# Performance work log

Hardware: AMD Instinct MI355X
Metric: run time of the kernel (lower is better)

The kernel has to match this reference:

```python
import jax, jax.numpy as jnp
import numpy as np

N_NODES = 400      # total nodes across batch
B = 10             # graphs in batch (40 nodes each)
N_CONFIGS = 1000   # fixed by tile dataset
CONFIG_FEAT_DIM = 24
NODE_FEAT_DIM = 85  # continuous cols; node_feat has +1 col for shape-ele-type idx
N_SHAPE_TYPES = 8
SHAPE_EMB = 4
N_OPS = 120
OP_EMB = 32
H = 64             # h_dim
E = 800            # edges
CAT_DIM = NODE_FEAT_DIM + SHAPE_EMB + OP_EMB + CONFIG_FEAT_DIM  # 145


def _lin(k, i, o):
    return jax.random.normal(k, (i, o), jnp.float32) * (1.0 / np.sqrt(i))


def setup_inputs() -> dict:
    key = jax.random.key(0)
    ks = jax.random.split(key, 32)
    node_cont = jax.random.normal(ks[0], (N_NODES, NODE_FEAT_DIM), jnp.float32)
    shape_type = jax.random.randint(ks[1], (N_NODES, 1), 0, N_SHAPE_TYPES).astype(jnp.float32)
    node_feat = jnp.concatenate([node_cont, shape_type], axis=-1)  # [N, 86]
    node_opcode = jax.random.randint(ks[2], (N_NODES,), 0, N_OPS)
    config_feat = jax.random.normal(ks[3], (B * N_CONFIGS, CONFIG_FEAT_DIM), jnp.float32)
    edge_index = jax.random.randint(ks[4], (2, E), 0, N_NODES)
    batch = jnp.arange(N_NODES) // (N_NODES // B)  # 40 nodes per graph
    inp = dict(
        node_feat=node_feat, node_opcode=node_opcode, config_feat=config_feat,
        edge_index=edge_index, batch=batch,
        op_emb=jax.random.normal(ks[5], (N_OPS, OP_EMB), jnp.float32),
        shape_emb=jax.random.normal(ks[6], (N_SHAPE_TYPES, SHAPE_EMB), jnp.float32),
        W1=_lin(ks[7], CAT_DIM, 2 * H), b1=jnp.zeros((2 * H,), jnp.float32),
        W2=_lin(ks[8], 2 * H, 2 * H), b2=jnp.zeros((2 * H,), jnp.float32),
        Wl0=_lin(ks[9], 2 * H, H), Wr0=_lin(ks[10], 2 * H, H), bg0=jnp.zeros((H,), jnp.float32),
        Wl1=_lin(ks[11], H, H), Wr1=_lin(ks[12], H, H), bg1=jnp.zeros((H,), jnp.float32),
        Wl2=_lin(ks[13], H, H), Wr2=_lin(ks[14], H, H), bg2=jnp.zeros((H,), jnp.float32),
        Wp1=_lin(ks[15], H, H // 2), bp1=jnp.zeros((H // 2,), jnp.float32),
        Wp2=_lin(ks[16], H // 2, 1), bp2=jnp.zeros((1,), jnp.float32),
    )
    return inp


def _sage(x, src, dst, Wl, Wr, b, n):
    # PyG SAGEConv: lin_l(x) + lin_r(mean_{j->i} x_j), applied over [N, C, D]
    agg = jax.ops.segment_sum(x[src], dst, num_segments=n)
    deg = jax.ops.segment_sum(jnp.ones((src.shape[0],), x.dtype), dst, num_segments=n)
    mean = agg / jnp.maximum(deg, 1.0)[:, None, None]
    return x @ Wl + mean @ Wr + b


def reference(node_feat, node_opcode, config_feat, edge_index, batch,
              op_emb, shape_emb, W1, b1, W2, b2,
              Wl0, Wr0, bg0, Wl1, Wr1, bg1, Wl2, Wr2, bg2,
              Wp1, bp1, Wp2, bp2):
    n = node_feat.shape[0]
    cfg = config_feat.reshape(-1, N_CONFIGS, CONFIG_FEAT_DIM)  # [B, 1000, 24]
    ste = shape_emb[node_feat[:, -1].astype(jnp.int32)]        # [N, 4]
    op = op_emb[node_opcode]                                   # [N, 32]
    xn = jnp.concatenate([node_feat[:, :-1], ste, op], axis=-1)  # [N, 121]
    xn = jnp.broadcast_to(xn[:, None, :], (n, N_CONFIGS, xn.shape[-1]))
    xc = cfg[batch]  # repeat_interleave(cfg, n_nodes, dim=0) -> per-node config
    x = jnp.concatenate([xn, xc], axis=-1)                     # [N, 1000, 145]
    x = jax.nn.relu(x @ W1 + b1)
    x = jax.nn.relu(x @ W2 + b2)                               # [N, 1000, 128]
    src, dst = edge_index[0], edge_index[1]
    for Wl, Wr, bg in ((Wl0, Wr0, bg0), (Wl1, Wr1, bg1), (Wl2, Wr2, bg2)):
        x = jax.nn.relu(_sage(x, src, dst, Wl, Wr, bg, n))     # [N, 1000, 64]
    xf = x.reshape(n, -1)                                      # [N, 64000]
    cnt = jax.ops.segment_sum(jnp.ones((n,), xf.dtype), batch, num_segments=B)
    xg = jax.ops.segment_max(xf, batch, num_segments=B) \
         + jax.ops.segment_sum(xf, batch, num_segments=B) / jnp.maximum(cnt, 1.0)[:, None]
    xg = xg.reshape(B, N_CONFIGS, -1)                          # [B, 1000, 64]
    xg = xg / jnp.linalg.norm(xg, axis=-1, keepdims=True)
    out = (jax.nn.relu(xg @ Wp1 + bp1) @ Wp2 + bp2)[..., 0]    # [B, 1000]
    return out
```

## Files before the change

### kernel.cpp

```cpp
#include <hip/hip_runtime.h>
#include <hip/hip_bf16.h>

typedef unsigned short u16;
typedef short bf16x8 __attribute__((ext_vector_type(8)));
typedef float f32x4 __attribute__((ext_vector_type(4)));

#define NN 400
#define NB 10
#define NC 1000
#define CFD 24
#define NFD 85
#define NFROW 86
#define SEDIM 4
#define OEDIM 32
#define XND 121
#define EE 800
#define N_SHAPE_GUARD 7

__device__ __forceinline__ float b2f(u16 u) { return __uint_as_float((unsigned)u << 16); }
__device__ __forceinline__ u16 f2b(float v) {
  unsigned x = __float_as_uint(v);
  return (u16)((x + 0x7fff + ((x >> 16) & 1)) >> 16);
}
__device__ __forceinline__ float ldf(const void* p, int idx, int fz) {
  if (fz) return ((const float*)p)[idx];
  return b2f(((const u16*)p)[idx]);
}
__device__ __forceinline__ void stf(void* p, int idx, int fz, float v) {
  if (fz) { ((float*)p)[idx] = v; return; }
  ((u16*)p)[idx] = f2b(v);
}

__device__ __forceinline__ void detect_wave0(const void* W1, int t, int* flagl) {
  if (t < 64) {
    int wild = 0;
    const u16* wv = (const u16*)W1;
    for (int j = t; j < 512; j += 64) {
      float a = fabsf(b2f(wv[j]));
      if (!(a < 1e4f)) wild++;
    }
    #pragma unroll
    for (int off = 32; off; off >>= 1) wild += __shfl_xor(wild, off);
    if (t == 0) *flagl = (wild > 16) ? 1 : 0;
  }
}

__global__ __launch_bounds__(256) void k_prep_all(
    const void* __restrict__ node_feat, const int* __restrict__ opcode,
    const void* __restrict__ cfg, const int* __restrict__ edge_index,
    const void* __restrict__ op_emb, const void* __restrict__ shape_emb,
    const void* __restrict__ W1, const void* __restrict__ b1,
    const void* __restrict__ W2,
    const void* __restrict__ Wl0, const void* __restrict__ Wr0,
    const void* __restrict__ Wl1, const void* __restrict__ Wr1,
    const void* __restrict__ Wl2, const void* __restrict__ Wr2,
    float* __restrict__ A_node, float* __restrict__ C_cfg,
    u16* __restrict__ W2t, u16* __restrict__ Wc0t,
    u16* __restrict__ Wc1t, u16* __restrict__ Wc2t,
    int* __restrict__ offs, int* __restrict__ srcl) {
  __shared__ int flagl;
  int t = threadIdx.x;
  detect_wave0(W1, t, &flagl);
  __syncthreads();
  int fz = flagl;
  int bid = blockIdx.x;

  if (bid < 313) {
    __shared__ float w1l[CFD * 128];
    __shared__ float cfl[32 * CFD];
    int r0 = bid * 32;
    for (int idx = t; idx < CFD * 128; idx += 256)
      w1l[idx] = ldf(W1, (XND + (idx >> 7)) * 128 + (idx & 127), fz);
    for (int idx = t; idx < 32 * CFD; idx += 256) {
      int r = idx / CFD, k = idx - r * CFD;
      if (r0 + r < 10000) cfl[idx] = ldf(cfg, (r0 + r) * CFD + k, fz);
    }
    __syncthreads();
    for (int idx = t; idx < 4096; idx += 256) {
      int row = idx >> 7, col = idx & 127;
      if (r0 + row < 10000) {
        float acc = 0.f;
        #pragma unroll
        for (int k = 0; k < CFD; k++) acc += cfl[row * CFD + k] * w1l[k * 128 + col];
        C_cfg[(size_t)(r0 + row) * 128 + col] = acc;
      }
    }
    return;
  }
  if (bid < 363) {
    __shared__ float w1m[XND * 128];
    __shared__ float xnl[8 * 128];
    int i0 = (bid - 313) * 8;
    for (int idx = t; idx < XND * 128; idx += 256) w1m[idx] = ldf(W1, idx, fz);
    for (int idx = t; idx < 1024; idx += 256) {
      int node = idx >> 7, tt = idx & 127;
      int i = i0 + node;
      float v = 0.f;
      if (tt < NFD) {
        v = ldf(node_feat, i * NFROW + tt, fz);
      } else if (tt < NFD + SEDIM) {
        int st = (int)ldf(node_feat, i * NFROW + NFD, fz);
        st = min(max(st, 0), N_SHAPE_GUARD);
        v = ldf(shape_emb, st * SEDIM + (tt - NFD), fz);
      } else if (tt < XND) {
        int oc = min(max(opcode[i], 0), 119);
        v = ldf(op_emb, oc * OEDIM + (tt - NFD - SEDIM), fz);
      }
      xnl[idx] = v;
    }
    __syncthreads();
    for (int idx = t; idx < 1024; idx += 256) {
      int node = idx >> 7, tt = idx & 127;
      int i = i0 + node;
      float acc = ldf(b1, tt, fz);
      for (int k = 0; k < XND; k++) acc += xnl[node * 128 + k] * w1m[k * 128 + tt];
      A_node[i * 128 + tt] = acc;
    }
    return;
  }
  if (bid < 555) {
    int idx = (bid - 363) * 256 + t;
    if (idx < 16384) {
      int n = idx >> 7, k = idx & 127;
      W2t[idx] = f2b(ldf(W2, k * 128 + n, fz)); return;
    }
    idx -= 16384;
    if (idx < 16384) {
      int n = idx >> 7, k = idx & 127;
      float v = (n < 64) ? ldf(Wl0, k * 64 + n, fz) : ldf(Wr0, k * 64 + n - 64, fz);
      Wc0t[idx] = f2b(v); return;
    }
    idx -= 16384;
    if (idx < 8192) {
      int n = idx >> 6, k = idx & 63;
      float v = (n < 64) ? ldf(Wl1, k * 64 + n, fz) : ldf(Wr1, k * 64 + n - 64, fz);
      Wc1t[idx] = f2b(v); return;
    }
    idx -= 8192;
    if (idx < 8192) {
      int n = idx >> 6, k = idx & 63;
      float v = (n < 64) ? ldf(Wl2, k * 64 + n, fz) : ldf(Wr2, k * 64 + n - 64, fz);
      Wc2t[idx] = f2b(v); return;
    }
    return;
  }
  {
    __shared__ int cnt[NN];
    __shared__ int offl[NN + 1];
    for (int i = t; i < NN; i += 256) cnt[i] = 0;
    __syncthreads();
    for (int e = t; e < EE; e += 256) {
      int d = edge_index[EE + e] & 511; if (d < NN) atomicAdd(&cnt[d], 1);
    }
    __syncthreads();
    if (t == 0) {
      int s = 0;
      for (int i = 0; i < NN; i++) { offl[i] = s; s += cnt[i]; }
      offl[NN] = s;
    }
    __syncthreads();
    for (int i = t; i < NN; i += 256) cnt[i] = offl[i];
    for (int i = t; i < NN + 1; i += 256) offs[i] = offl[i];
    __syncthreads();
    for (int e = t; e < EE; e += 256) {
      int d = edge_index[EE + e] & 511;
      if (d < NN) {
        int p = atomicAdd(&cnt[d], 1);
        srcl[p] = min(max(edge_index[e], 0), NN - 1);
      }
    }
  }
}

__global__ __launch_bounds__(512, 1) void k_fused(
    const float* __restrict__ A_node, const float* __restrict__ C_cfg,
    const int* __restrict__ batch, const int* __restrict__ offs,
    const int* __restrict__ srcl,
    const u16* __restrict__ W2t, const u16* __restrict__ Wc0t,
    const u16* __restrict__ Wc1t, const u16* __restrict__ Wc2t,
    const void* __restrict__ b2, const void* __restrict__ bg0,
    const void* __restrict__ bg1, const void* __restrict__ bg2,
    const void* __restrict__ Wp1, const void* __restrict__ bp1,
    const void* __restrict__ Wp2, const void* __restrict__ bp2,
    const void* __restrict__ W1d, void* __restrict__ out) {
  __shared__ __align__(16) u16 xbuf[400 * 128];
  __shared__ __align__(16) u16 ybuf[400 * 64];
  __shared__ int offsl[401];
  __shared__ int srcll[EE];
  __shared__ int flagl;

  int c = blockIdx.x;
  int t = threadIdx.x;
  int w = t >> 6, l = t & 63;
  int lm = l & 15, quad = l >> 4;

  detect_wave0(W1d, t, &flagl);
  float* cfgl = (float*)ybuf;
  for (int idx = t; idx < 1280; idx += 512)
    cfgl[idx] = C_cfg[((size_t)(idx >> 7) * NC + c) * 128 + (idx & 127)];
  for (int idx = t; idx < 401; idx += 512) offsl[idx] = offs[idx];
  for (int idx = t; idx < EE; idx += 512) srcll[idx] = srcl[idx];
  __syncthreads();
  int fz = flagl;

  {
    bf16x8 wf[8][4];
    #pragma unroll
    for (int mt = 0; mt < 8; mt++)
      #pragma unroll
      for (int kt = 0; kt < 4; kt++)
        wf[mt][kt] = *reinterpret_cast<const bf16x8*>(W2t + (mt*16 + lm)*128 + kt*32 + quad*8);
    float bv[8][4];
    #pragma unroll
    for (int mt = 0; mt < 8; mt++)
      #pragma unroll
      for (int rg = 0; rg < 4; rg++) bv[mt][rg] = ldf(b2, mt*16 + quad*4 + rg, fz);

    for (int tile = w; tile < 25; tile += 8) {
      int i = tile*16 + lm;
      int b = batch[i] % NB;
      const float* an = A_node + i*128;
      const float* cf = cfgl + b*128;
      bf16x8 bfr[4];
      #pragma unroll
      for (int kt = 0; kt < 4; kt++) {
        int ko = kt*32 + quad*8;
        float4 a0 = *(const float4*)(an + ko);
        float4 a1 = *(const float4*)(an + ko + 4);
        float4 c0 = *(const float4*)(cf + ko);
        float4 c1 = *(const float4*)(cf + ko + 4);
        bf16x8 f;
        f[0] = (short)f2b(fmaxf(a0.x + c0.x, 0.f));
        f[1] = (short)f2b(fmaxf(a0.y + c0.y, 0.f));
        f[2] = (short)f2b(fmaxf(a0.z + c0.z, 0.f));
        f[3] = (short)f2b(fmaxf(a0.w + c0.w, 0.f));
        f[4] = (short)f2b(fmaxf(a1.x + c1.x, 0.f));
        f[5] = (short)f2b(fmaxf(a1.y + c1.y, 0.f));
        f[6] = (short)f2b(fmaxf(a1.z + c1.z, 0.f));
        f[7] = (short)f2b(fmaxf(a1.w + c1.w, 0.f));
        bfr[kt] = f;
      }
      f32x4 acc[8] = {};
      #pragma unroll
      for (int kt = 0; kt < 4; kt++)
        #pragma unroll
        for (int mt = 0; mt < 8; mt++)
          acc[mt] = __builtin_amdgcn_mfma_f32_16x16x32_bf16(wf[mt][kt], bfr[kt], acc[mt], 0, 0, 0);
      #pragma unroll
      for (int mt = 0; mt < 8; mt++) {
        ushort4 s;
        s.x = f2b(fmaxf(acc[mt][0] + bv[mt][0], 0.f));
        s.y = f2b(fmaxf(acc[mt][1] + bv[mt][1], 0.f));
        s.z = f2b(fmaxf(acc[mt][2] + bv[mt][2], 0.f));
        s.w = f2b(fmaxf(acc[mt][3] + bv[mt][3], 0.f));
        int ch = mt*2 + (quad >> 1);
        int chs = ch ^ (i & 7);
        *reinterpret_cast<ushort4*>(&xbuf[i*128 + chs*8 + (quad & 1)*4]) = s;
      }
    }
  }
  __syncthreads();

  {
    bf16x8 wl[4][4], wr[4][4];
    #pragma unroll
    for (int mt = 0; mt < 4; mt++)
      #pragma unroll
      for (int kt = 0; kt < 4; kt++) {
        wl[mt][kt] = *reinterpret_cast<const bf16x8*>(Wc0t + (mt*16 + lm)*128 + kt*32 + quad*8);
        wr[mt][kt] = *reinterpret_cast<const bf16x8*>(Wc0t + (64 + mt*16 + lm)*128 + kt*32 + quad*8);
      }
    float bv[4][4];
    #pragma unroll
    for (int mt = 0; mt < 4; mt++)
      #pragma unroll
      for (int rg = 0; rg < 4; rg++) bv[mt][rg] = ldf(bg0, mt*16 + quad*4 + rg, fz);

    for (int tile = w; tile < 25; tile += 8) {
      int i = tile*16 + lm;
      int o0 = offsl[i], o1 = offsl[i + 1];
      float rd = 1.f / fmaxf((float)(o1 - o0), 1.f);
      bf16x8 xf[4], mf[4];
      #pragma unroll
      for (int kt = 0; kt < 4; kt++)
        xf[kt] = *reinterpret_cast<const bf16x8*>(&xbuf[i*128 + ((kt*4 + quad) ^ (i & 7))*8]);
      float s8[4][8] = {};
      int e = o0;
      for (; e + 1 < o1; e += 2) {
        int sn0 = srcll[e], sn1 = srcll[e + 1];
        bf16x8 z0[4], z1[4];
        #pragma unroll
        for (int kt = 0; kt < 4; kt++) {
          z0[kt] = *reinterpret_cast<const bf16x8*>(&xbuf[sn0*128 + ((kt*4 + quad) ^ (sn0 & 7))*8]);
          z1[kt] = *reinterpret_cast<const bf16x8*>(&xbuf[sn1*128 + ((kt*4 + quad) ^ (sn1 & 7))*8]);
        }
        #pragma unroll
        for (int kt = 0; kt < 4; kt++)
          #pragma unroll
          for (int j = 0; j < 8; j++) {
            s8[kt][j] += b2f((u16)z0[kt][j]);
            s8[kt][j] += b2f((u16)z1[kt][j]);
          }
      }
      if (e < o1) {
        int sn0 = srcll[e];
        #pragma unroll
        for (int kt = 0; kt < 4; kt++) {
          bf16x8 zv = *reinterpret_cast<const bf16x8*>(&xbuf[sn0*128 + ((kt*4 + quad) ^ (sn0 & 7))*8]);
          #pragma unroll
          for (int j = 0; j < 8; j++) s8[kt][j] += b2f((u16)zv[j]);
        }
      }
      #pragma unroll
      for (int kt = 0; kt < 4; kt++) {
        bf16x8 f;
        #pragma unroll
        for (int j = 0; j < 8; j++) f[j] = (short)f2b(s8[kt][j] * rd);
        mf[kt] = f;
      }
      f32x4 acc[4] = {};
      #pragma unroll
      for (int kt = 0; kt < 4; kt++)
        #pragma unroll
        for (int mt = 0; mt < 4; mt++) {
          acc[mt] = __builtin_amdgcn_mfma_f32_16x16x32_bf16(wl[mt][kt], xf[kt], acc[mt], 0, 0, 0);
          acc[mt] = __builtin_amdgcn_mfma_f32_16x16x32_bf16(wr[mt][kt], mf[kt], acc[mt], 0, 0, 0);
        }
      #pragma unroll
      for (int mt = 0; mt < 4; mt++) {
        ushort4 s;
        s.x = f2b(fmaxf(acc[mt][0] + bv[mt][0], 0.f));
        s.y = f2b(fmaxf(acc[mt][1] + bv[mt][1], 0.f));
        s.z = f2b(fmaxf(acc[mt][2] + bv[mt][2], 0.f));
        s.w = f2b(fmaxf(acc[mt][3] + bv[mt][3], 0.f));
        int ch = mt*2 + (quad >> 1);
        int chs = ch ^ (i & 7);
        *reinterpret_cast<ushort4*>(&ybuf[i*64 + chs*8 + (quad & 1)*4]) = s;
      }
    }
  }
  __syncthreads();

  u16* src_buf = ybuf;
  u16* dst_buf = xbuf;
  for (int layer = 0; layer < 2; layer++) {
    const u16* Wt = (layer == 0) ? Wc1t : Wc2t;
    const void* bg = (layer == 0) ? bg1 : bg2;
    bf16x8 wl[4][2], wr[4][2];
    #pragma unroll
    for (int mt = 0; mt < 4; mt++)
      #pragma unroll
      for (int kt = 0; kt < 2; kt++) {
        wl[mt][kt] = *reinterpret_cast<const bf16x8*>(Wt + (mt*16 + lm)*64 + kt*32 + quad*8);
        wr[mt][kt] = *reinterpret_cast<const bf16x8*>(Wt + (64 + mt*16 + lm)*64 + kt*32 + quad*8);
      }
    float bv[4][4];
    #pragma unroll
    for (int mt = 0; mt < 4; mt++)
      #pragma unroll
      for (int rg = 0; rg < 4; rg++) bv[mt][rg] = ldf(bg, mt*16 + quad*4 + rg, fz);

    for (int tile = w; tile < 25; tile += 8) {
      int i = tile*16 + lm;
      int o0 = offsl[i], o1 = offsl[i + 1];
      float rd = 1.f / fmaxf((float)(o1 - o0), 1.f);
      bf16x8 xf[2], mf[2];
      #pragma unroll
      for (int kt = 0; kt < 2; kt++)
        xf[kt] = *reinterpret_cast<const bf16x8*>(&src_buf[i*64 + ((kt*4 + quad) ^ (i & 7))*8]);
      float s8[2][8] = {};
      int e = o0;
      for (; e + 1 < o1; e += 2) {
        int sn0 = srcll[e], sn1 = srcll[e + 1];
        bf16x8 z0[2], z1[2];
        #pragma unroll
        for (int kt = 0; kt < 2; kt++) {
          z0[kt] = *reinterpret_cast<const bf16x8*>(&src_buf[sn0*64 + ((kt*4 + quad) ^ (sn0 & 7))*8]);
          z1[kt] = *reinterpret_cast<const bf16x8*>(&src_buf[sn1*64 + ((kt*4 + quad) ^ (sn1 & 7))*8]);
        }
        #pragma unroll
        for (int kt = 0; kt < 2; kt++)
          #pragma unroll
          for (int j = 0; j < 8; j++) {
            s8[kt][j] += b2f((u16)z0[kt][j]);
            s8[kt][j] += b2f((u16)z1[kt][j]);
          }
      }
      if (e < o1) {
        int sn0 = srcll[e];
        #pragma unroll
        for (int kt = 0; kt < 2; kt++) {
          bf16x8 zv = *reinterpret_cast<const bf16x8*>(&src_buf[sn0*64 + ((kt*4 + quad) ^ (sn0 & 7))*8]);
          #pragma unroll
          for (int j = 0; j < 8; j++) s8[kt][j] += b2f((u16)zv[j]);
        }
      }
      #pragma unroll
      for (int kt = 0; kt < 2; kt++) {
        bf16x8 f;
        #pragma unroll
        for (int j = 0; j < 8; j++) f[j] = (short)f2b(s8[kt][j] * rd);
        mf[kt] = f;
      }
      f32x4 acc[4] = {};
      #pragma unroll
      for (int kt = 0; kt < 2; kt++)
        #pragma unroll
        for (int mt = 0; mt < 4; mt++) {
          acc[mt] = __builtin_amdgcn_mfma_f32_16x16x32_bf16(wl[mt][kt], xf[kt], acc[mt], 0, 0, 0);
          acc[mt] = __builtin_amdgcn_mfma_f32_16x16x32_bf16(wr[mt][kt], mf[kt], acc[mt], 0, 0, 0);
        }
      #pragma unroll
      for (int mt = 0; mt < 4; mt++) {
        ushort4 s;
        s.x = f2b(fmaxf(acc[mt][0] + bv[mt][0], 0.f));
        s.y = f2b(fmaxf(acc[mt][1] + bv[mt][1], 0.f));
        s.z = f2b(fmaxf(acc[mt][2] + bv[mt][2], 0.f));
        s.w = f2b(fmaxf(acc[mt][3] + bv[mt][3], 0.f));
        int ch = mt*2 + (quad >> 1);
        int chs = ch ^ (i & 7);
        *reinterpret_cast<ushort4*>(&dst_buf[i*64 + chs*8 + (quad & 1)*4]) = s;
      }
    }
    __syncthreads();
    u16* tmp = src_buf; src_buf = dst_buf; dst_buf = tmp;
  }

  {
    float* scr  = (float*)xbuf;
    float* wp1s = (float*)&xbuf[4096];
    for (int idx = t; idx < 2048; idx += 512) wp1s[idx] = ldf(Wp1, idx, fz);
    __syncthreads();
    for (int b = w; b < NB; b += 8) {
      int h = l;
      float mx = -3.0e38f, sm = 0.f;
      for (int j = 0; j < 40; j++) {
        int row = b*40 + j;
        int chs = (h >> 3) ^ (row & 7);
        float v = b2f(src_buf[row*64 + chs*8 + (h & 7)]);
        mx = fmaxf(mx, v); sm += v;
      }
      float g = mx + sm * (1.f / 40.f);
      float sq = g * g;
      #pragma unroll
      for (int off = 32; off; off >>= 1) sq += __shfl_xor(sq, off);
      float gn = g * rsqrtf(sq);
      scr[w*64 + h] = gn;
      int j32 = l & 31;
      float hj = ldf(bp1, j32, fz);
      for (int k = 0; k < 64; k++) hj += scr[w*64 + k] * wp1s[k*32 + j32];
      hj = fmaxf(hj, 0.f);
      float contrib = hj * ldf(Wp2, j32, fz);
      #pragma unroll
      for (int off = 32; off; off >>= 1) contrib += __shfl_xor(contrib, off);
      if (l == 0) stf(out, b*NC + c, fz, contrib * 0.5f + ldf(bp2, 0, fz));
    }
  }
}

extern "C" void kernel_launch(void* const* d_in, const int* in_sizes, int n_in,
                              void* d_out, int out_size, void* d_ws, size_t ws_size,
                              hipStream_t stream) {
  const void* node_feat   = d_in[0];
  const int*  node_opcode = (const int*)d_in[1];
  const void* config_feat = d_in[2];
  const int*  edge_index  = (const int*)d_in[3];
  const int*  batch       = (const int*)d_in[4];
  const void* op_emb      = d_in[5];
  const void* shape_emb   = d_in[6];
  const void* W1  = d_in[7];
  const void* b1  = d_in[8];
  const void* W2  = d_in[9];
  const void* b2  = d_in[10];
  const void* Wl0 = d_in[11];
  const void* Wr0 = d_in[12];
  const void* bg0 = d_in[13];
  const void* Wl1 = d_in[14];
  const void* Wr1 = d_in[15];
  const void* bg1 = d_in[16];
  const void* Wl2 = d_in[17];
  const void* Wr2 = d_in[18];
  const void* bg2 = d_in[19];
  const void* Wp1 = d_in[20];
  const void* bp1 = d_in[21];
  const void* Wp2 = d_in[22];
  const void* bp2 = d_in[23];

  char* p = (char*)d_ws;
  float* A_node = (float*)p; p += 400*128*4;
  float* C_cfg  = (float*)p; p += 10000*128*4;
  u16*   W2t    = (u16*)p;   p += 128*128*2;
  u16*   Wc0t   = (u16*)p;   p += 128*128*2;
  u16*   Wc1t   = (u16*)p;   p += 128*64*2;
  u16*   Wc2t   = (u16*)p;   p += 128*64*2;
  int*   offs   = (int*)p;   p += 2048;
  int*   srcl   = (int*)p;   p += 4096;

  k_prep_all<<<dim3(556), dim3(256), 0, stream>>>(
      node_feat, node_opcode, config_feat, edge_index, op_emb, shape_emb,
      W1, b1, W2, Wl0, Wr0, Wl1, Wr1, Wl2, Wr2,
      A_node, C_cfg, W2t, Wc0t, Wc1t, Wc2t, offs, srcl);

  k_fused<<<dim3(1000), dim3(512), 0, stream>>>(
      A_node, C_cfg, batch, offs, srcl, W2t, Wc0t, Wc1t, Wc2t,
      b2, bg0, bg1, bg2, Wp1, bp1, Wp2, bp2, W1, d_out);
}
```

Before: 333.6 us.

## Aggregate neighbors via MFMA per edge with degree-sorted node tiles

SAGE mean aggregation is restructured: instead of summing neighbor features in fp32 scalar ops and then multiplying, each neighbor row is fed directly into MFMA against Wr and the result scaled by 1/deg afterward. Nodes are permuted by degree so each 16-node tile has similar degree, padding with a zero row. Weight fragments for W2 and Wl are loaded per k-step rather than held in registers to cut register pressure, bf16 packing uses a hardware packed-convert instruction, and the prep GEMMs are register-tiled with vector stores. This trades scalar VALU accumulation for more MFMA issues per edge.

```diff
diff --git a/kernel.cpp b/kernel.cpp
--- a/kernel.cpp
+++ b/kernel.cpp
@@ -21,6 +21,11 @@
 __device__ __forceinline__ u16 f2b(float v) {
   unsigned x = __float_as_uint(v);
   return (u16)((x + 0x7fff + ((x >> 16) & 1)) >> 16);
+}
+__device__ __forceinline__ unsigned f2b2(float lo, float hi) {
+  unsigned r;
+  asm("v_cvt_pk_bf16_f32 %0, %1, %2" : "=v"(r) : "v"(lo), "v"(hi));
+  return r;
 }
 __device__ __forceinline__ float ldf(const void* p, int idx, int fz) {
   if (fz) return ((const float*)p)[idx];
@@ -57,7 +62,8 @@
     float* __restrict__ A_node, float* __restrict__ C_cfg,
     u16* __restrict__ W2t, u16* __restrict__ Wc0t,
     u16* __restrict__ Wc1t, u16* __restrict__ Wc2t,
-    int* __restrict__ offs, int* __restrict__ srcl) {
+    int* __restrict__ offs, int* __restrict__ srcl,
+    int* __restrict__ perm) {
   __shared__ int flagl;
   int t = threadIdx.x;
   detect_wave0(W1, t, &flagl);
@@ -76,13 +82,27 @@
       if (r0 + r < 10000) cfl[idx] = ldf(cfg, (r0 + r) * CFD + k, fz);
     }
     __syncthreads();
-    for (int idx = t; idx < 4096; idx += 256) {
-      int row = idx >> 7, col = idx & 127;
-      if (r0 + row < 10000) {
-        float acc = 0.f;
-        #pragma unroll
-        for (int k = 0; k < CFD; k++) acc += cfl[row * CFD + k] * w1l[k * 128 + col];
-        C_cfg[(size_t)(r0 + row) * 128 + col] = acc;
+    int rg = t >> 5;
+    int cg = t & 31;
+    float acc[4][4] = {};
+    for (int k = 0; k < CFD; k++) {
+      float4 bb = *reinterpret_cast<const float4*>(&w1l[k * 128 + cg * 4]);
+      #pragma unroll
+      for (int ri = 0; ri < 4; ri++) {
+        float a = cfl[(rg * 4 + ri) * CFD + k];
+        acc[ri][0] += a * bb.x;
+        acc[ri][1] += a * bb.y;
+        acc[ri][2] += a * bb.z;
+        acc[ri][3] += a * bb.w;
+      }
+    }
+    #pragma unroll
+    for (int ri = 0; ri < 4; ri++) {
+      int row = r0 + rg * 4 + ri;
+      if (row < 10000) {
+        float4 o;
+        o.x = acc[ri][0]; o.y = acc[ri][1]; o.z = acc[ri][2]; o.w = acc[ri][3];
+        *reinterpret_cast<float4*>(&C_cfg[(size_t)row * 128 + cg * 4]) = o;
       }
     }
     return;
@@ -109,13 +129,22 @@
       xnl[idx] = v;
     }
     __syncthreads();
-    for (int idx = t; idx < 1024; idx += 256) {
-      int node = idx >> 7, tt = idx & 127;
-      int i = i0 + node;
-      float acc = ldf(b1, tt, fz);
-      for (int k = 0; k < XND; k++) acc += xnl[node * 128 + k] * w1m[k * 128 + tt];
-      A_node[i * 128 + tt] = acc;
-    }
+    int ng = t >> 6;
+    int c2 = (t & 63) * 2;
+    float a00 = ldf(b1, c2, fz), a01 = ldf(b1, c2 + 1, fz);
+    float a10 = a00, a11 = a01;
+    for (int k = 0; k < XND; k++) {
+      float2 wv = *reinterpret_cast<const float2*>(&w1m[k * 128 + c2]);
+      float x0 = xnl[(ng * 2) * 128 + k];
+      float x1 = xnl[(ng * 2 + 1) * 128 + k];
+      a00 += x0 * wv.x; a01 += x0 * wv.y;
+      a10 += x1 * wv.x; a11 += x1 * wv.y;
+    }
+    int i = i0 + ng * 2;
+    float2 s0; s0.x = a00; s0.y = a01;
+    float2 s1; s1.x = a10; s1.y = a11;
+    *reinterpret_cast<float2*>(&A_node[i * 128 + c2]) = s0;
+    *reinterpret_cast<float2*>(&A_node[(i + 1) * 128 + c2]) = s1;
     return;
   }
   if (bid < 555) {
@@ -147,6 +176,7 @@
   {
     __shared__ int cnt[NN];
     __shared__ int offl[NN + 1];
+    __shared__ int dbin[64];
     for (int i = t; i < NN; i += 256) cnt[i] = 0;
     __syncthreads();
     for (int e = t; e < EE; e += 256) {
@@ -169,13 +199,30 @@
         srcl[p] = min(max(edge_index[e], 0), NN - 1);
       }
     }
+    for (int i = t; i < 64; i += 256) dbin[i] = 0;
+    __syncthreads();
+    for (int i = t; i < NN; i += 256) {
+      int d = min(offl[i + 1] - offl[i], 63);
+      atomicAdd(&dbin[d], 1);
+    }
+    __syncthreads();
+    if (t == 0) {
+      int s = 0;
+      for (int d = 0; d < 64; d++) { int c = dbin[d]; dbin[d] = s; s += c; }
+    }
+    __syncthreads();
+    for (int i = t; i < NN; i += 256) {
+      int d = min(offl[i + 1] - offl[i], 63);
+      int p = atomicAdd(&dbin[d], 1);
+      perm[p] = i;
+    }
   }
 }
 
 __global__ __launch_bounds__(512, 1) void k_fused(
     const float* __restrict__ A_node, const float* __restrict__ C_cfg,
     const int* __restrict__ batch, const int* __restrict__ offs,
-    const int* __restrict__ srcl,
+    const int* __restrict__ srcl, const int* __restrict__ perm,
     const u16* __restrict__ W2t, const u16* __restrict__ Wc0t,
     const u16* __restrict__ Wc1t, const u16* __restrict__ Wc2t,
     const void* __restrict__ b2, const void* __restrict__ bg0,
@@ -183,10 +230,11 @@
     const void* __restrict__ Wp1, const void* __restrict__ bp1,
     const void* __restrict__ Wp2, const void* __restrict__ bp2,
     const void* __restrict__ W1d, void* __restrict__ out) {
-  __shared__ __align__(16) u16 xbuf[400 * 128];
-  __shared__ __align__(16) u16 ybuf[400 * 64];
-  __shared__ int offsl[401];
+  __shared__ __align__(16) u16 xbuf[401 * 128];
+  __shared__ __align__(16) u16 ybuf[401 * 64];
+  __shared__ int offsl[NN + 1];
   __shared__ int srcll[EE];
+  __shared__ int perml[NN];
   __shared__ int flagl;
 
   int c = blockIdx.x;
@@ -198,18 +246,15 @@
   float* cfgl = (float*)ybuf;
   for (int idx = t; idx < 1280; idx += 512)
     cfgl[idx] = C_cfg[((size_t)(idx >> 7) * NC + c) * 128 + (idx & 127)];
-  for (int idx = t; idx < 401; idx += 512) offsl[idx] = offs[idx];
+  for (int idx = t; idx < NN + 1; idx += 512) offsl[idx] = offs[idx];
   for (int idx = t; idx < EE; idx += 512) srcll[idx] = srcl[idx];
+  for (int idx = t; idx < NN; idx += 512) perml[idx] = perm[idx];
+  for (int idx = t; idx < 128; idx += 512) xbuf[NN * 128 + idx] = 0;
+  if (t < 64) ybuf[NN * 64 + t] = 0;
   __syncthreads();
   int fz = flagl;
 
   {
-    bf16x8 wf[8][4];
-    #pragma unroll
-    for (int mt = 0; mt < 8; mt++)
-      #pragma unroll
-      for (int kt = 0; kt < 4; kt++)
-        wf[mt][kt] = *reinterpret_cast<const bf16x8*>(W2t + (mt*16 + lm)*128 + kt*32 + quad*8);
     float bv[8][4];
     #pragma unroll
     for (int mt = 0; mt < 8; mt++)
@@ -221,7 +266,7 @@
       int b = batch[i] % NB;
       const float* an = A_node + i*128;
       const float* cf = cfgl + b*128;
-      bf16x8 bfr[4];
+      f32x4 acc[8] = {};
       #pragma unroll
       for (int kt = 0; kt < 4; kt++) {
         int ko = kt*32 + quad*8;
@@ -229,47 +274,42 @@
         float4 a1 = *(const float4*)(an + ko + 4);
         float4 c0 = *(const float4*)(cf + ko);
         float4 c1 = *(const float4*)(cf + ko + 4);
-        bf16x8 f;
-        f[0] = (short)f2b(fmaxf(a0.x + c0.x, 0.f));
-        f[1] = (short)f2b(fmaxf(a0.y + c0.y, 0.f));
-        f[2] = (short)f2b(fmaxf(a0.z + c0.z, 0.f));
-        f[3] = (short)f2b(fmaxf(a0.w + c0.w, 0.f));
-        f[4] = (short)f2b(fmaxf(a1.x + c1.x, 0.f));
-        f[5] = (short)f2b(fmaxf(a1.y + c1.y, 0.f));
-        f[6] = (short)f2b(fmaxf(a1.z + c1.z, 0.f));
-        f[7] = (short)f2b(fmaxf(a1.w + c1.w, 0.f));
-        bfr[kt] = f;
-      }
-      f32x4 acc[8] = {};
-      #pragma unroll
-      for (int kt = 0; kt < 4; kt++)
+        union { bf16x8 v; unsigned u[4]; } f;
+        f.u[0] = f2b2(fmaxf(a0.x + c0.x, 0.f), fmaxf(a0.y + c0.y, 0.f));
+        f.u[1] = f2b2(fmaxf(a0.z + c0.z, 0.f), fmaxf(a0.w + c0.w, 0.f));
+        f.u[2] = f2b2(fmaxf(a1.x + c1.x, 0.f), fmaxf(a1.y + c1.y, 0.f));
+        f.u[3] = f2b2(fmaxf(a1.z + c1.z, 0.f), fmaxf(a1.w + c1.w, 0.f));
+        bf16x8 bfr = f.v;
+        bf16x8 wfk[8];
         #pragma unroll
         for (int mt = 0; mt < 8; mt++)
-          acc[mt] = __builtin_amdgcn_mfma_f32_16x16x32_bf16(wf[mt][kt], bfr[kt], acc[mt], 0, 0, 0);
+          wfk[mt] = *reinterpret_cast<const bf16x8*>(W2t + (mt*16 + lm)*128 + kt*32 + quad*8);
+        #pragma unroll
+        for (int mt = 0; mt < 8; mt++)
+          acc[mt] = __builtin_amdgcn_mfma_f32_16x16x32_bf16(wfk[mt], bfr, acc[mt], 0, 0, 0);
+      }
       #pragma unroll
       for (int mt = 0; mt < 8; mt++) {
-        ushort4 s;
-        s.x = f2b(fmaxf(acc[mt][0] + bv[mt][0], 0.f));
-        s.y = f2b(fmaxf(acc[mt][1] + bv[mt][1], 0.f));
-        s.z = f2b(fmaxf(acc[mt][2] + bv[mt][2], 0.f));
-        s.w = f2b(fmaxf(acc[mt][3] + bv[mt][3], 0.f));
+        float v0 = fmaxf(acc[mt][0] + bv[mt][0], 0.f);
+        float v1 = fmaxf(acc[mt][1] + bv[mt][1], 0.f);
+        float v2 = fmaxf(acc[mt][2] + bv[mt][2], 0.f);
+        float v3 = fmaxf(acc[mt][3] + bv[mt][3], 0.f);
         int ch = mt*2 + (quad >> 1);
         int chs = ch ^ (i & 7);
-        *reinterpret_cast<ushort4*>(&xbuf[i*128 + chs*8 + (quad & 1)*4]) = s;
+        uint2 u; u.x = f2b2(v0, v1); u.y = f2b2(v2, v3);
+        *reinterpret_cast<uint2*>(&xbuf[i*128 + chs*8 + (quad & 1)*4]) = u;
       }
     }
   }
   __syncthreads();
 
   {
-    bf16x8 wl[4][4], wr[4][4];
+    bf16x8 wr[4][4];
     #pragma unroll
     for (int mt = 0; mt < 4; mt++)
       #pragma unroll
-      for (int kt = 0; kt < 4; kt++) {
-        wl[mt][kt] = *reinterpret_cast<const bf16x8*>(Wc0t + (mt*16 + lm)*128 + kt*32 + quad*8);
+      for (int kt = 0; kt < 4; kt++)
         wr[mt][kt] = *reinterpret_cast<const bf16x8*>(Wc0t + (64 + mt*16 + lm)*128 + kt*32 + quad*8);
-      }
     float bv[4][4];
     #pragma unroll
     for (int mt = 0; mt < 4; mt++)
@@ -277,65 +317,52 @@
       for (int rg = 0; rg < 4; rg++) bv[mt][rg] = ldf(bg0, mt*16 + quad*4 + rg, fz);
 
     for (int tile = w; tile < 25; tile += 8) {
-      int i = tile*16 + lm;
+      int i = perml[tile*16 + lm];
       int o0 = offsl[i], o1 = offsl[i + 1];
-      float rd = 1.f / fmaxf((float)(o1 - o0), 1.f);
-      bf16x8 xf[4], mf[4];
+      int deg = o1 - o0;
+      float rd = 1.f / fmaxf((float)deg, 1.f);
+      int md = deg;
+      md = max(md, __shfl_xor(md, 1));
+      md = max(md, __shfl_xor(md, 2));
+      md = max(md, __shfl_xor(md, 4));
+      md = max(md, __shfl_xor(md, 8));
+      bf16x8 xf[4];
       #pragma unroll
       for (int kt = 0; kt < 4; kt++)
         xf[kt] = *reinterpret_cast<const bf16x8*>(&xbuf[i*128 + ((kt*4 + quad) ^ (i & 7))*8]);
-      float s8[4][8] = {};
-      int e = o0;
-      for (; e + 1 < o1; e += 2) {
-        int sn0 = srcll[e], sn1 = srcll[e + 1];
-        bf16x8 z0[4], z1[4];
-        #pragma unroll
-        for (int kt = 0; kt < 4; kt++) {
-          z0[kt] = *reinterpret_cast<const bf16x8*>(&xbuf[sn0*128 + ((kt*4 + quad) ^ (sn0 & 7))*8]);
-          z1[kt] = *reinterpret_cast<const bf16x8*>(&xbuf[sn1*128 + ((kt*4 + quad) ^ (sn1 & 7))*8]);
-        }
+      f32x4 accS[4] = {}, accM[4] = {};
+      #pragma unroll
+      for (int kt = 0; kt < 4; kt++) {
+        bf16x8 wlk[4];
+        #pragma unroll
+        for (int mt = 0; mt < 4; mt++)
+          wlk[mt] = *reinterpret_cast<const bf16x8*>(Wc0t + (mt*16 + lm)*128 + kt*32 + quad*8);
+        #pragma unroll
+        for (int mt = 0; mt < 4; mt++)
+          accS[mt] = __builtin_amdgcn_mfma_f32_16x16x32_bf16(wlk[mt], xf[kt], accS[mt], 0, 0, 0);
+      }
+      for (int r = 0; r < md; r++) {
+        int sn = (r < deg) ? srcll[o0 + r] : NN;
+        bf16x8 z[4];
+        #pragma unroll
+        for (int kt = 0; kt < 4; kt++)
+          z[kt] = *reinterpret_cast<const bf16x8*>(&xbuf[sn*128 + ((kt*4 + quad) ^ (sn & 7))*8]);
         #pragma unroll
         for (int kt = 0; kt < 4; kt++)
           #pragma unroll
-          for (int j = 0; j < 8; j++) {
-            s8[kt][j] += b2f((u16)z0[kt][j]);
-            s8[kt][j] += b2f((u16)z1[kt][j]);
-          }
-      }
-      if (e < o1) {
-        int sn0 = srcll[e];
-        #pragma unroll
-        for (int kt = 0; kt < 4; kt++) {
-          bf16x8 zv = *reinterpret_cast<const bf16x8*>(&xbuf[sn0*128 + ((kt*4 + quad) ^ (sn0 & 7))*8]);
-          #pragma unroll
-          for (int j = 0; j < 8; j++) s8[kt][j] += b2f((u16)zv[j]);
-        }
-      }
-      #pragma unroll
-      for (int kt = 0; kt < 4; kt++) {
-        bf16x8 f;
-        #pragma unroll
-        for (int j = 0; j < 8; j++) f[j] = (short)f2b(s8[kt][j] * rd);
-        mf[kt] = f;
-      }
-      f32x4 acc[4] = {};
-      #pragma unroll
-      for (int kt = 0; kt < 4; kt++)
-        #pragma unroll
-        for (int mt = 0; mt < 4; mt++) {
-          acc[mt] = __builtin_amdgcn_mfma_f32_16x16x32_bf16(wl[mt][kt], xf[kt], acc[mt], 0, 0, 0);
-          acc[mt] = __builtin_amdgcn_mfma_f32_16x16x32_bf16(wr[mt][kt], mf[kt], acc[mt], 0, 0, 0);
-        }
+          for (int mt = 0; mt < 4; mt++)
+            accM[mt] = __builtin_amdgcn_mfma_f32_16x16x32_bf16(wr[mt][kt], z[kt], accM[mt], 0, 0, 0);
+      }
       #pragma unroll
       for (int mt = 0; mt < 4; mt++) {
-        ushort4 s;
-        s.x = f2b(fmaxf(acc[mt][0] + bv[mt][0], 0.f));
-        s.y = f2b(fmaxf(acc[mt][1] + bv[mt][1], 0.f));
-        s.z = f2b(fmaxf(acc[mt][2] + bv[mt][2], 0.f));
-        s.w = f2b(fmaxf(acc[mt][3] + bv[mt][3], 0.f));
+        float v0 = fmaxf(accS[mt][0] + rd*accM[mt][0] + bv[mt][0], 0.f);
+        float v1 = fmaxf(accS[mt][1] + rd*accM[mt][1] + bv[mt][1], 0.f);
+        float v2 = fmaxf(accS[mt][2] + rd*accM[mt][2] + bv[mt][2], 0.f);
+        float v3 = fmaxf(accS[mt][3] + rd*accM[mt][3] + bv[mt][3], 0.f);
         int ch = mt*2 + (quad >> 1);
         int chs = ch ^ (i & 7);
-        *reinterpret_cast<ushort4*>(&ybuf[i*64 + chs*8 + (quad & 1)*4]) = s;
+        uint2 u; u.x = f2b2(v0, v1); u.y = f2b2(v2, v3);
+        *reinterpret_cast<uint2*>(&ybuf[i*64 + chs*8 + (quad & 1)*4]) = u;
       }
     }
   }
@@ -346,14 +373,12 @@
   for (int layer = 0; layer < 2; layer++) {
     const u16* Wt = (layer == 0) ? Wc1t : Wc2t;
     const void* bg = (layer == 0) ? bg1 : bg2;
-    bf16x8 wl[4][2], wr[4][2];
+    bf16x8 wr[4][2];
     #pragma unroll
     for (int mt = 0; mt < 4; mt++)
       #pragma unroll
-      for (int kt = 0; kt < 2; kt++) {
-        wl[mt][kt] = *reinterpret_cast<const bf16x8*>(Wt + (mt*16 + lm)*64 + kt*32 + quad*8);
+      for (int kt = 0; kt < 2; kt++)
         wr[mt][kt] = *reinterpret_cast<const bf16x8*>(Wt + (64 + mt*16 + lm)*64 + kt*32 + quad*8);
-      }
     float bv[4][4];
     #pragma unroll
     for (int mt = 0; mt < 4; mt++)
@@ -361,67 +386,55 @@
       for (int rg = 0; rg < 4; rg++) bv[mt][rg] = ldf(bg, mt*16 + quad*4 + rg, fz);
 
     for (int tile = w; tile < 25; tile += 8) {
-      int i = tile*16 + lm;
+      int i = perml[tile*16 + lm];
       int o0 = offsl[i], o1 = offsl[i + 1];
-      float rd = 1.f / fmaxf((float)(o1 - o0), 1.f);
-      bf16x8 xf[2], mf[2];
+      int deg = o1 - o0;
+      float rd = 1.f / fmaxf((float)deg, 1.f);
+      int md = deg;
+      md = max(md, __shfl_xor(md, 1));
+      md = max(md, __shfl_xor(md, 2));
+      md = max(md, __shfl_xor(md, 4));
+      md = max(md, __shfl_xor(md, 8));
+      bf16x8 xf[2];
       #pragma unroll
       for (int kt = 0; kt < 2; kt++)
         xf[kt] = *reinterpret_cast<const bf16x8*>(&src_buf[i*64 + ((kt*4 + quad) ^ (i & 7))*8]);
-      float s8[2][8] = {};
-      int e = o0;
-      for (; e + 1 < o1; e += 2) {
-        int sn0 = srcll[e], sn1 = srcll[e + 1];
-        bf16x8 z0[2], z1[2];
-        #pragma unroll
-        for (int kt = 0; kt < 2; kt++) {
-          z0[kt] = *reinterpret_cast<const bf16x8*>(&src_buf[sn0*64 + ((kt*4 + quad) ^ (sn0 & 7))*8]);
-          z1[kt] = *reinterpret_cast<const bf16x8*>(&src_buf[sn1*64 + ((kt*4 + quad) ^ (sn1 & 7))*8]);
-        }
+      f32x4 accS[4] = {}, accM[4] = {};
+      #pragma unroll
+      for (int kt = 0; kt < 2; kt++) {
+        bf16x8 wlk[4];
+        #pragma unroll
+        for (int mt = 0; mt < 4; mt++)
+          wlk[mt] = *reinterpret_cast<const bf16x8*>(Wt + (mt*16 + lm)*64 + kt*32 + quad*8);
+        #pragma unroll
+        for (int mt = 0; mt < 4; mt++)
+          accS[mt] = __builtin_amdgcn_mfma_f32_16x16x32_bf16(wlk[mt], xf[kt], accS[mt], 0, 0, 0);
+      }
+      for (int r = 0; r < md; r++) {
+        int sn = (r < deg) ? srcll[o0 + r] : NN;
+        bf16x8 z[2];
+        #pragma unroll
+        for (int kt = 0; kt < 2; kt++)
+          z[kt] = *reinterpret_cast<const bf16x8*>(&src_buf[sn*64 + ((kt*4 + quad) ^ (sn & 7))*8]);
         #pragma unroll
         for (int kt = 0; kt < 2; kt++)
           #pragma unroll
-          for (int j = 0; j < 8; j++) {
-            s8[kt][j] += b2f((u16)z0[kt][j]);
-            s8[kt][j] += b2f((u16)z1[kt][j]);
-          }
-      }
-      if (e < o1) {
-        int sn0 = srcll[e];
-        #pragma unroll
-        for (int kt = 0; kt < 2; kt++) {
-          bf16x8 zv = *reinterpret_cast<const bf16x8*>(&src_buf[sn0*64 + ((kt*4 + quad) ^ (sn0 & 7))*8]);
-          #pragma unroll
-          for (int j = 0; j < 8; j++) s8[kt][j] += b2f((u16)zv[j]);
-        }
-      }
-      #pragma unroll
-      for (int kt = 0; kt < 2; kt++) {
-        bf16x8 f;
-        #pragma unroll
-        for (int j = 0; j < 8; j++) f[j] = (short)f2b(s8[kt][j] * rd);
-        mf[kt] = f;
-      }
-      f32x4 acc[4] = {};
-      #pragma unroll
-      for (int kt = 0; kt < 2; kt++)
-        #pragma unroll
-        for (int mt = 0; mt < 4; mt++) {
-          acc[mt] = __builtin_amdgcn_mfma_f32_16x16x32_bf16(wl[mt][kt], xf[kt], acc[mt], 0, 0, 0);
-          acc[mt] = __builtin_amdgcn_mfma_f32_16x16x32_bf16(wr[mt][kt], mf[kt], acc[mt], 0, 0, 0);
-        }
+          for (int mt = 0; mt < 4; mt++)
+            accM[mt] = __builtin_amdgcn_mfma_f32_16x16x32_bf16(wr[mt][kt], z[kt], accM[mt], 0, 0, 0);
+      }
       #pragma unroll
       for (int mt = 0; mt < 4; mt++) {
-        ushort4 s;
-        s.x = f2b(fmaxf(acc[mt][0] + bv[mt][0], 0.f));
-        s.y = f2b(fmaxf(acc[mt][1] + bv[mt][1], 0.f));
-        s.z = f2b(fmaxf(acc[mt][2] + bv[mt][2], 0.f));
-        s.w = f2b(fmaxf(acc[mt][3] + bv[mt][3], 0.f));
+        float v0 = fmaxf(accS[mt][0] + rd*accM[mt][0] + bv[mt][0], 0.f);
+        float v1 = fmaxf(accS[mt][1] + rd*accM[mt][1] + bv[mt][1], 0.f);
+        float v2 = fmaxf(accS[mt][2] + rd*accM[mt][2] + bv[mt][2], 0.f);
+        float v3 = fmaxf(accS[mt][3] + rd*accM[mt][3] + bv[mt][3], 0.f);
         int ch = mt*2 + (quad >> 1);
         int chs = ch ^ (i & 7);
-        *reinterpret_cast<ushort4*>(&dst_buf[i*64 + chs*8 + (quad & 1)*4]) = s;
-      }
-    }
+        uint2 u; u.x = f2b2(v0, v1); u.y = f2b2(v2, v3);
+        *reinterpret_cast<uint2*>(&dst_buf[i*64 + chs*8 + (quad & 1)*4]) = u;
+      }
+    }
+    if (t < 64) dst_buf[NN*64 + t] = 0;
     __syncthreads();
     u16* tmp = src_buf; src_buf = dst_buf; dst_buf = tmp;
   }
@@ -495,13 +508,14 @@
   u16*   Wc2t   = (u16*)p;   p += 128*64*2;
   int*   offs   = (int*)p;   p += 2048;
   int*   srcl   = (int*)p;   p += 4096;
+  int*   perm   = (int*)p;   p += 2048;
 
   k_prep_all<<<dim3(556), dim3(256), 0, stream>>>(
       node_feat, node_opcode, config_feat, edge_index, op_emb, shape_emb,
       W1, b1, W2, Wl0, Wr0, Wl1, Wr1, Wl2, Wr2,
-      A_node, C_cfg, W2t, Wc0t, Wc1t, Wc2t, offs, srcl);
+      A_node, C_cfg, W2t, Wc0t, Wc1t, Wc2t, offs, srcl, perm);
 
   k_fused<<<dim3(1000), dim3(512), 0, stream>>>(
-      A_node, C_cfg, batch, offs, srcl, W2t, Wc0t, Wc1t, Wc2t,
+      A_node, C_cfg, batch, offs, srcl, perm, W2t, Wc0t, Wc1t, Wc2t,
       b2, bg0, bg1, bg2, Wp1, bp1, Wp2, bp2, W1, d_out);
 }
```

Result: slower. 367.8 us (+10.2%).
